# Kernel tuning notes

Hardware: AMD Instinct MI355X
Metric: run time of the kernel (lower is better)

The kernel has to match this reference:

```python
import jax, jax.numpy as jnp
import numpy as np

Lx, Ly, D, P = 4, 5, 4, 2
DEPTH = 5
TAU = 0.1
N = Lx * Ly
B = 64


def setup_inputs() -> dict:
    key = jax.random.key(0)
    k1, k2, k3 = jax.random.split(key, 3)
    # PEPS site tensors: [Lx, Ly, phys, up, down, left, right]; boundary bonds sliced to dim 1 at use.
    peps = jax.random.normal(k1, (Lx, Ly, P, D, D, D, D), dtype=jnp.float32) * 0.5
    # Two-site Trotter gate: expm(-tau * h) for a random symmetric two-body term h (4x4).
    h = jax.random.normal(k2, (4, 4), dtype=jnp.float32)
    h = 0.5 * (h + h.T)
    w, v = jnp.linalg.eigh(h)
    gate = (v * jnp.exp(-TAU * w)) @ v.T  # [4,4]
    x = jax.random.randint(k3, (B, N), 0, 2, dtype=jnp.int32)
    return {"x": x, "peps": peps, "gate": gate}


def _slice_boundary(site, i, j):
    # site: [p, u, d, l, r]; open boundary -> bond dim 1 on lattice edges
    if i == 0:
        site = site[:, :1]
    if i == Lx - 1:
        site = site[:, :, :1]
    if j == 0:
        site = site[:, :, :, :1]
    if j == Ly - 1:
        site = site[..., :1]
    return site


def _peps_statevector(peps):
    # Exact contraction of the open-boundary PEPS to the full 2^N statevector.
    rows = []
    for i in range(Lx):
        T = jnp.ones((1, 1, 1, 1), dtype=peps.dtype)  # [Pphys, Uup, Ddown, l]
        for j in range(Ly):
            s = _slice_boundary(peps[i, j], i, j)
            T = jnp.einsum('PUDl,pudlr->PpUuDdr', T, s)
            Pn, p, U, u, Dn, d, r = T.shape
            T = T.reshape(Pn * p, U * u, Dn * d, r)
        rows.append(T[..., 0])  # [2^Ly, up_bonds, down_bonds]
    S = jnp.ones((1, 1), dtype=peps.dtype)  # [Pphys, down_bonds]
    for row in rows:
        S = jnp.einsum('PU,QUD->PQD', S, row)
        a, b, c = S.shape
        S = S.reshape(a * b, c)
    return S[:, 0]  # [2^N]


def _apply_gate(psi, g, a, b):
    # g: [2,2,2,2] = gate[o1,o2,i1,i2]; psi: (2,)*N
    out = jnp.tensordot(g, psi, axes=([2, 3], [a, b]))
    return jnp.moveaxis(out, (0, 1), (a, b))


def _bonds():
    horiz = [((i, j), (i, j + 1)) for i in range(Lx) for j in range(Ly - 1)]
    vert = [((i, j), (i + 1, j)) for i in range(Lx - 1) for j in range(Ly)]
    return horiz + vert


def reference(x, peps, gate):
    psi = _peps_statevector(peps).reshape((2,) * N)
    g = gate.reshape(2, 2, 2, 2)
    bonds = _bonds()
    for _ in range(DEPTH):
        for (i1, j1), (i2, j2) in bonds:
            psi = _apply_gate(psi, g, i1 * Ly + j1, i2 * Ly + j2)
    psi = psi.reshape(-1)
    pw = 2 ** jnp.arange(N - 1, -1, -1, dtype=jnp.int32)
    idx = (x * pw).sum(axis=1)
    return psi[idx]  # [B] amplitudes
```

## Files before the change

kernel.cpp:

```cpp
#include <hip/hip_runtime.h>


#define PAD(i) ((i) + (((i) >> 4) << 2))
#define PIDX(i,j,p,u,d,l,r) (((((((i)*5+(j))*2+(p))*4+(u))*4+(d))*4+(l))*4+(r))

typedef float v4f __attribute__((ext_vector_type(4)));

static constexpr int COL0  = 0;
static constexpr int COL1  = 4096;
static constexpr int COL2  = COL1 + 1048576;
static constexpr int COL3  = COL2 + 1048576;
static constexpr int COL4  = COL3 + 1048576;
static constexpr int M01TO = COL4 + 4096;
static constexpr int M34TO = M01TO + 65536;
static constexpr int T12TO = M34TO + 65536;
static constexpr int PSIO  = T12TO + 1048576;
static constexpr int CNTO  = PSIO + 1048576;

__device__ __forceinline__ float agl(const float* p) {
  return __hip_atomic_load(p, __ATOMIC_RELAXED, __HIP_MEMORY_SCOPE_AGENT);
}
__device__ __forceinline__ void cohload1(const float* p, v4f& a) {
  asm volatile("global_load_dwordx4 %0, %1, off sc0 sc1"
               : "=&v"(a) : "v"(p) : "memory");
}
__device__ __forceinline__ void cohload2(const float* p0, const float* p1,
                                         v4f& a, v4f& b) {
  asm volatile(
      "global_load_dwordx4 %0, %2, off sc0 sc1\n\t"
      "global_load_dwordx4 %1, %3, off sc0 sc1\n\t"
      "s_waitcnt vmcnt(0)"
      : "=&v"(a), "=&v"(b)
      : "v"(p0), "v"(p1)
      : "memory");
}
__device__ __forceinline__ void cohstore(float* p, v4f v) {
  asm volatile("global_store_dwordx4 %0, %1, off sc0 sc1"
               :
               : "v"(p), "v"(v)
               : "memory");
}
__device__ __forceinline__ void cohstore1(float* p, float v) {
  asm volatile("global_store_dword %0, %1, off sc0 sc1"
               :
               : "v"(p), "v"(v)
               : "memory");
}
__device__ __forceinline__ void vmdrain() {
  asm volatile("s_waitcnt vmcnt(0)" ::: "memory");
}
__device__ __forceinline__ void vmw8() {
  asm volatile("s_waitcnt vmcnt(8)" ::: "memory");
  __builtin_amdgcn_sched_barrier(0);
}
__device__ __forceinline__ void vmw0() {
  asm volatile("s_waitcnt vmcnt(0)" ::: "memory");
  __builtin_amdgcn_sched_barrier(0);
}

__device__ __forceinline__ void gridbar(int* cnts, int gen) {
  vmdrain();
  __syncthreads();
  if (threadIdx.x == 0) {
    int* gc = cnts + (blockIdx.x >> 4) * 64;
    int* root = cnts + 1024;
    int prev = __hip_atomic_fetch_add(gc, 1, __ATOMIC_RELAXED,
                                      __HIP_MEMORY_SCOPE_AGENT);
    if ((prev & 15) == 15)
      __hip_atomic_fetch_add(root, 1, __ATOMIC_RELAXED,
                             __HIP_MEMORY_SCOPE_AGENT);
    while (__hip_atomic_load(root, __ATOMIC_RELAXED,
                             __HIP_MEMORY_SCOPE_AGENT) < gen * 16) {
      __builtin_amdgcn_s_sleep(2);
    }
  }
  __syncthreads();
}

__device__ __forceinline__ void coh_gemm(const float* Bb, const float* Ar,
                                         v4f acc[4]) {
  v4f pa0, pa1, pa2, pa3, pa4, pa5, pa6, pa7;
  v4f pb0, pb1, pb2, pb3, pb4, pb5, pb6, pb7;
#define ISSUE8(buf, base)                                                      \
  cohload1(Bb + ((base) + 0) * 256, buf##0);                                   \
  cohload1(Bb + ((base) + 1) * 256, buf##1);                                   \
  cohload1(Bb + ((base) + 2) * 256, buf##2);                                   \
  cohload1(Bb + ((base) + 3) * 256, buf##3);                                   \
  cohload1(Bb + ((base) + 4) * 256, buf##4);                                   \
  cohload1(Bb + ((base) + 5) * 256, buf##5);                                   \
  cohload1(Bb + ((base) + 6) * 256, buf##6);                                   \
  cohload1(Bb + ((base) + 7) * 256, buf##7)
#define FMA8(buf, base)                                                        \
  {                                                                            \
    _Pragma("unroll") for (int r = 0; r < 4; ++r) {                            \
      acc[r] += buf##0 * Ar[r * 256 + (base) + 0];                             \
      acc[r] += buf##1 * Ar[r * 256 + (base) + 1];                             \
      acc[r] += buf##2 * Ar[r * 256 + (base) + 2];                             \
      acc[r] += buf##3 * Ar[r * 256 + (base) + 3];                             \
      acc[r] += buf##4 * Ar[r * 256 + (base) + 4];                             \
      acc[r] += buf##5 * Ar[r * 256 + (base) + 5];                             \
      acc[r] += buf##6 * Ar[r * 256 + (base) + 6];                             \
      acc[r] += buf##7 * Ar[r * 256 + (base) + 7];                             \
    }                                                                          \
  }
  ISSUE8(pa, 0);
#pragma unroll
  for (int cp = 0; cp < 16; ++cp) {
    ISSUE8(pb, cp * 16 + 8);
    vmw8();
    FMA8(pa, cp * 16);
    if (cp < 15) {
      ISSUE8(pa, cp * 16 + 16);
      vmw8();
    } else {
      vmw0();
    }
    FMA8(pb, cp * 16 + 8);
  }
#undef ISSUE8
#undef FMA8
}

__device__ __forceinline__ void stage8k(const float* gsrc, float* lds, int t) {
  v4f v0, v1, v2, v3;
  cohload1(gsrc + (0 * 512 + t) * 4, v0);
  cohload1(gsrc + (1 * 512 + t) * 4, v1);
  cohload1(gsrc + (2 * 512 + t) * 4, v2);
  cohload1(gsrc + (3 * 512 + t) * 4, v3);
  vmw0();
  *(v4f*)&lds[(0 * 512 + t) * 4] = v0;
  *(v4f*)&lds[(1 * 512 + t) * 4] = v1;
  *(v4f*)&lds[(2 * 512 + t) * 4] = v2;
  *(v4f*)&lds[(3 * 512 + t) * 4] = v3;
}

template <int NB, int HI, int LO>
__device__ __forceinline__ void gate2(float* x, const float* __restrict__ g) {
  constexpr int H = 1 << HI, L = 1 << LO, N = 1 << NB;
#pragma unroll
  for (int o = 0; o < N; ++o) {
    if (o & (H | L)) continue;
    float v0 = x[o], v1 = x[o + L], v2 = x[o + H], v3 = x[o + H + L];
    x[o]         = g[0]  * v0 + g[1]  * v1 + g[2]  * v2 + g[3]  * v3;
    x[o + L]     = g[4]  * v0 + g[5]  * v1 + g[6]  * v2 + g[7]  * v3;
    x[o + H]     = g[8]  * v0 + g[9]  * v1 + g[10] * v2 + g[11] * v3;
    x[o + H + L] = g[12] * v0 + g[13] * v1 + g[14] * v2 + g[15] * v3;
  }
}

template <int ST>
__device__ __forceinline__ void vxf(float* s, const float* __restrict__ g, int b) {
  float x[16];
#pragma unroll
  for (int m = 0; m < 16; ++m) x[m] = s[PAD(b + m * ST)];
  gate2<4, 3, 2>(x, g);
  gate2<4, 2, 1>(x, g);
  gate2<4, 1, 0>(x, g);
#pragma unroll
  for (int m = 0; m < 16; ++m) s[PAD(b + m * ST)] = x[m];
}

template <int B2, int B1, int B0>
__device__ __forceinline__ void bondpair(float* s, const float* __restrict__ g,
                                         int t) {
  constexpr int MASK = (1 << B2) | (1 << B1) | (1 << B0);
  int b = 0, rem = t;
#pragma unroll
  for (int p = 0; p < 12; ++p) {
    if (!((MASK >> p) & 1)) {
      b |= (rem & 1) << p;
      rem >>= 1;
    }
  }
  float x[8];
#pragma unroll
  for (int m = 0; m < 8; ++m) {
    int off = ((m >> 2) & 1) * (1 << B2) + ((m >> 1) & 1) * (1 << B1) +
              (m & 1) * (1 << B0);
    x[m] = s[PAD(b + off)];
  }
  gate2<3, 2, 1>(x, g);
  gate2<3, 1, 0>(x, g);
#pragma unroll
  for (int m = 0; m < 8; ++m) {
    int off = ((m >> 2) & 1) * (1 << B2) + ((m >> 1) & 1) * (1 << B1) +
              (m & 1) * (1 << B0);
    s[PAD(b + off)] = x[m];
  }
}

__global__ __launch_bounds__(512) void k_all(const float* __restrict__ peps,
                                             const int* __restrict__ x,
                                             const float* __restrict__ gate,
                                             float* __restrict__ ws,
                                             float* __restrict__ out,
                                             int* __restrict__ cnt) {
  __shared__ float sm[12320];
  const int t = threadIdx.x;
  const int b = blockIdx.x;
  const int cg = t & 63;
  float* psi = ws + PSIO;
  int gen = 0;

  if (b < 192) {
    float* p01 = sm;
    float* p23 = sm + 4096;
    int col = 1 + (b >> 6);
    int pb = b & 63;
#pragma unroll
    for (int k = 0; k < 8; ++k) {
      int e = k * 512 + t;
      int r12 = e & 15, l12 = (e >> 4) & 15, d2 = (e >> 8) & 3, p = e >> 10;
      int l1 = l12 >> 2, l2 = l12 & 3, r1 = r12 >> 2, r2 = r12 & 3;
      float s01 = 0.f, s23 = 0.f;
#pragma unroll
      for (int d = 0; d < 4; ++d) {
        s01 += peps[PIDX(0, col, (p >> 1), 0, d, l1, r1)] *
               peps[PIDX(1, col, (p & 1), d, d2, l2, r2)];
        s23 += peps[PIDX(2, col, (p >> 1), d2, d, l1, r1)] *
               peps[PIDX(3, col, (p & 1), d, 0, l2, r2)];
      }
      p01[e] = s01;
      p23[e] = s23;
    }
    __syncthreads();
    const int coloffs[3] = {COL1, COL2, COL3};
    float* outc = ws + coloffs[col - 1];
#pragma unroll
    for (int pp = 0; pp < 2; ++pp) {
      int part = pb * 2 + pp;
#pragma unroll
      for (int k = 0; k < 4; ++k) {
        int eq = part * 8192 + (k * 512 + t) * 4;
        int r34b = eq & 15;
        int r12 = (eq >> 4) & 15, l34 = (eq >> 8) & 15, l12 = (eq >> 12) & 15;
        int p = eq >> 16;
        int pa = p >> 2, pbv = p & 3;
        v4f acc = {0.f, 0.f, 0.f, 0.f};
#pragma unroll
        for (int d2 = 0; d2 < 4; ++d2) {
          float a01 = p01[((((pa * 4 + d2) << 4) | l12) << 4) | r12];
          const float4 b4 =
              *(const float4*)&p23[((((pbv * 4 + d2) << 4) | l34) << 4) | r34b];
          acc.x += a01 * b4.x;
          acc.y += a01 * b4.y;
          acc.z += a01 * b4.z;
          acc.w += a01 * b4.w;
        }
        cohstore(&outc[eq], acc);
      }
    }
  } else if (b < 194) {
    float* p01 = sm;
    float* p23 = sm + 4096;
    int col = (b == 192) ? 0 : 4;
    const int lsh = (col == 0) ? 0 : 2;
    const int rsh = (col == 4) ? 0 : 2;
    const int ldim = 1 << lsh, rdim = 1 << rsh;
    const int LLB = 2 * lsh, RRB = 2 * rsh;
    const int LL = 1 << LLB, RR = 1 << RRB;
    int n12 = (LL * RR) << 4;
    for (int e = t; e < n12; e += 512) {
      int r12 = e & (RR - 1);
      int l12 = (e >> RRB) & (LL - 1);
      int d2 = (e >> (RRB + LLB)) & 3;
      int p = e >> (RRB + LLB + 2);
      int l1 = l12 >> lsh, l2 = l12 & (ldim - 1);
      int r1 = r12 >> rsh, r2 = r12 & (rdim - 1);
      float s01 = 0.f, s23 = 0.f;
      for (int d = 0; d < 4; ++d) {
        s01 += peps[PIDX(0, col, (p >> 1), 0, d, l1, r1)] *
               peps[PIDX(1, col, (p & 1), d, d2, l2, r2)];
        s23 += peps[PIDX(2, col, (p >> 1), d2, d, l1, r1)] *
               peps[PIDX(3, col, (p & 1), d, 0, l2, r2)];
      }
      p01[e] = s01;
      p23[e] = s23;
    }
    __syncthreads();
    const int LB = 2 * LLB, RB = 2 * RRB;
    int total = 16 << (LB + RB);
    float* outc = ws + ((col == 0) ? COL0 : COL4);
    for (int e = t; e < total; e += 512) {
      int r = e & ((1 << RB) - 1);
      int l = (e >> RB) & ((1 << LB) - 1);
      int p = e >> (RB + LB);
      int r34 = r & (RR - 1), r12 = r >> RRB;
      int l34 = l & (LL - 1), l12 = l >> LLB;
      int pa = p >> 2, pbv = p & 3;
      float sacc = 0.f;
      for (int d2 = 0; d2 < 4; ++d2) {
        sacc += p01[((((pa * 4 + d2) << LLB) | l12) << RRB) | r12] *
                p23[((((pbv * 4 + d2) << LLB) | l34) << RRB) | r34];
      }
      cohstore1(&outc[e], sacc);
    }
  }
  gridbar(cnt, ++gen);

  {
    float* c3buf = sm;
    float* c4buf = sm + 4112;
    float* col0l = sm + 8224;
    const float* col3 = ws + COL3;
    const float* col4 = ws + COL4;
    const float* col0g = ws + COL0;
    const int L3 = b;
    if (t < 256) {
      float v3[16], v4[16];
#pragma unroll
      for (int k = 0; k < 16; ++k) {
        v4[k] = agl(&col4[k * 256 + t]);
        v3[k] = agl(&col3[k * 65536 + L3 * 256 + t]);
      }
#pragma unroll
      for (int k = 0; k < 16; ++k) {
        c4buf[k * 257 + t] = v4[k];
        c3buf[k * 257 + t] = v3[k];
      }
    } else if (b < 16) {
      int tt = t - 256;
#pragma unroll
      for (int k = 0; k < 16; ++k) col0l[k * 256 + tt] = agl(&col0g[k * 256 + tt]);
    }
    __syncthreads();
    if (t < 256) {
      int c3 = t >> 4, c4 = t & 15;
      float acc = 0.f;
      for (int B = 0; B < 256; ++B)
        acc += c3buf[c3 * 257 + B] * c4buf[c4 * 257 + B];
      cohstore1(&(ws + M34TO)[L3 * 256 + t], acc);
    } else if (b < 16) {
      int rg = (t >> 6) & 3;
      v4f acc[4] = {};
      coh_gemm(ws + COL1 + b * 65536 + cg * 4, &col0l[rg * 4 * 256], acc);
      float* m01p = ws + M01TO;
#pragma unroll
      for (int r = 0; r < 4; ++r)
        cohstore(&m01p[((rg * 4 + r) * 16 + b) * 256 + cg * 4], acc[r]);
    }
  }
  gridbar(cnt, ++gen);

  if (b < 128) {
    float* A = sm;
    int c2 = b & 15, hb = b >> 4;
    stage8k(ws + M01TO + hb * 8192, A, t);
    __syncthreads();
    int rg = t >> 6;
    v4f acc[4] = {};
    coh_gemm(ws + COL2 + c2 * 65536 + cg * 4, &A[rg * 4 * 256], acc);
    float* t012p = ws + T12TO;
#pragma unroll
    for (int r = 0; r < 4; ++r)
      cohstore(&t012p[c2 * 65536 + (hb * 32 + rg * 4 + r) * 256 + cg * 4],
               acc[r]);
  }
  gridbar(cnt, ++gen);

  if (b < 128) {
    float* A = sm;
    float* S = sm;
    {
      v4f v0, v1, v2, v3;
      const float* t012p = ws + T12TO;
      int f0 = (0 * 512 + t) * 4, f1 = (1 * 512 + t) * 4;
      int f2 = (2 * 512 + t) * 4, f3 = (3 * 512 + t) * 4;
      cohload1(t012p + (((f0 >> 8) & 15) * 65536 + (2 * b + (f0 >> 12)) * 256 +
                        (f0 & 255)), v0);
      cohload1(t012p + (((f1 >> 8) & 15) * 65536 + (2 * b + (f1 >> 12)) * 256 +
                        (f1 & 255)), v1);
      cohload1(t012p + (((f2 >> 8) & 15) * 65536 + (2 * b + (f2 >> 12)) * 256 +
                        (f2 & 255)), v2);
      cohload1(t012p + (((f3 >> 8) & 15) * 65536 + (2 * b + (f3 >> 12)) * 256 +
                        (f3 & 255)), v3);
      vmw0();
      *(v4f*)&A[f0] = v0;
      *(v4f*)&A[f1] = v1;
      *(v4f*)&A[f2] = v2;
      *(v4f*)&A[f3] = v3;
    }
    __syncthreads();
    int rg = t >> 6;
    v4f acc[4] = {};
    coh_gemm(ws + M34TO + cg * 4, &A[rg * 4 * 256], acc);
    __syncthreads();
#pragma unroll
    for (int r = 0; r < 4; ++r) {
      int ri = rg * 4 + r;
      int sb = (ri >> 4) * 4112 + (ri & 15) * 257 + cg * 4;
      S[sb + 0] = acc[r].x;
      S[sb + 1] = acc[r].y;
      S[sb + 2] = acc[r].z;
      S[sb + 3] = acc[r].w;
    }
    __syncthreads();
    int tid = t & 255, tgl = t >> 8;
    int c3 = tid >> 4, c2v = tid & 15;
    int tg = 2 * b + tgl;
    int base = c3 * 65536 + (tg >> 4) * 256 + (tg & 15) * 16 + c2v;
#pragma unroll
    for (int v = 0; v < 16; ++v)
      cohstore1(&psi[base + v * 4096], S[tgl * 4112 + c2v * 257 + c3 * 16 + v]);
  }
  gridbar(cnt, ++gen);

  float g[16];
#pragma unroll
  for (int i = 0; i < 16; ++i) g[i] = gate[i];
  float* s = sm;

  for (int it = 0; it < 5; ++it) {
    {
      int f0 = t * 4, f1 = (512 + t) * 4;
      v4f a, c;
      cohload2(psi + b * 4096 + f0, psi + b * 4096 + f1, a, c);
      *(v4f*)(s + PAD(f0)) = a;
      *(v4f*)(s + PAD(f1)) = c;
    }
    __syncthreads();
    bondpair<8, 4, 0>(s, g, t);
    __syncthreads();
    bondpair<9, 5, 1>(s, g, t);
    __syncthreads();
    bondpair<10, 6, 2>(s, g, t);
    __syncthreads();
    bondpair<11, 7, 3>(s, g, t);
    __syncthreads();
    if (t < 256) vxf<256>(s, g, t);
    __syncthreads();
    if (t < 256) vxf<16>(s, g, ((t >> 4) << 8) | (t & 15));
    __syncthreads();
    {
      int f0 = t * 4, f1 = (512 + t) * 4;
      cohstore(psi + b * 4096 + f0, *(const v4f*)(s + PAD(f0)));
      cohstore(psi + b * 4096 + f1, *(const v4f*)(s + PAD(f1)));
    }
    gridbar(cnt, ++gen);

    {
      int f0 = t * 4, f1 = (512 + t) * 4;
      int a0 = (f0 >> 8) * 65536 + ((f0 >> 4) & 15) * 4096 + b * 16 + (f0 & 15);
      int a1 = (f1 >> 8) * 65536 + ((f1 >> 4) & 15) * 4096 + b * 16 + (f1 & 15);
      v4f a, c;
      cohload2(psi + a0, psi + a1, a, c);
      *(v4f*)(s + PAD(f0)) = a;
      *(v4f*)(s + PAD(f1)) = c;
    }
    __syncthreads();
    bondpair<0, 8, 4>(s, g, t);
    __syncthreads();
    bondpair<1, 9, 5>(s, g, t);
    __syncthreads();
    bondpair<2, 10, 6>(s, g, t);
    __syncthreads();
    bondpair<3, 11, 7>(s, g, t);
    __syncthreads();
    if (t < 256) vxf<1>(s, g, t * 16);
    __syncthreads();
    if (t < 256) vxf<256>(s, g, t);
    __syncthreads();
    if (t < 256) vxf<16>(s, g, ((t >> 4) << 8) | (t & 15));
    __syncthreads();
    if (it == 4) {
      if (t < 64) {
        int idx = 0;
#pragma unroll
        for (int q = 0; q < 20; ++q) {
          int i = q / 5, j = q % 5;
          int pos = (j == 0) ? (11 - i)
                   : (j == 1) ? (7 - i)
                   : (j == 2) ? (3 - i)
                   : (j == 3) ? (19 - i)
                              : (15 - i);
          idx |= x[t * 20 + q] << pos;
        }
        if (((idx >> 4) & 255) == b) {
          int local = ((idx >> 16) & 15) * 256 + ((idx >> 12) & 15) * 16 +
                      (idx & 15);
          out[t] = s[PAD(local)];
        }
      }
    } else {
      int f0 = t * 4, f1 = (512 + t) * 4;
      int a0 = (f0 >> 8) * 65536 + ((f0 >> 4) & 15) * 4096 + b * 16 + (f0 & 15);
      int a1 = (f1 >> 8) * 65536 + ((f1 >> 4) & 15) * 4096 + b * 16 + (f1 & 15);
      cohstore(psi + a0, *(const v4f*)(s + PAD(f0)));
      cohstore(psi + a1, *(const v4f*)(s + PAD(f1)));
      gridbar(cnt, ++gen);
    }
  }
}

extern "C" void kernel_launch(void* const* d_in, const int* in_sizes, int n_in,
                              void* d_out, int out_size, void* d_ws, size_t ws_size,
                              hipStream_t stream) {
  const int* x = (const int*)d_in[0];
  const float* peps = (const float*)d_in[1];
  const float* gate = (const float*)d_in[2];
  float* ws = (float*)d_ws;
  float* out = (float*)d_out;
  int* cnt = (int*)(ws + CNTO);

  hipMemsetAsync((void*)cnt, 0, 1088 * sizeof(int), stream);

  k_all<<<256, 512, 0, stream>>>(peps, x, gate, ws, out, cnt);
}
```

Before: 212.9 us.

## Spread contraction GEMM stages across all blocks with smaller output tiles

Reworks the M01, T012 and final psi-assembly stages so that every block in the grid takes part, where before only 16 or 128 blocks did. The M01 stage becomes a per-block LDS dot-product using a staged slice of column 1. The later GEMMs use a new two-row-per-thread variant with vectorized LDS reads and padded strides, and psi is written with vector stores. The aim is to cut idle blocks and per-block serial GEMM length between grid barriers, at the cost of more redundant staging loads and more LDS per block.

```diff
diff --git a/kernel.cpp b/kernel.cpp
--- a/kernel.cpp
+++ b/kernel.cpp
@@ -77,8 +77,9 @@
   __syncthreads();
 }
 
-__device__ __forceinline__ void coh_gemm(const float* Bb, const float* Ar,
-                                         v4f acc[4]) {
+__device__ __forceinline__ void coh_gemm2(const float* Bb, const float* Ar0,
+                                          const float* Ar1, v4f& acc0,
+                                          v4f& acc1) {
   v4f pa0, pa1, pa2, pa3, pa4, pa5, pa6, pa7;
   v4f pb0, pb1, pb2, pb3, pb4, pb5, pb6, pb7;
 #define ISSUE8(buf, base)                                                      \
@@ -92,16 +93,18 @@
   cohload1(Bb + ((base) + 7) * 256, buf##7)
 #define FMA8(buf, base)                                                        \
   {                                                                            \
-    _Pragma("unroll") for (int r = 0; r < 4; ++r) {                            \
-      acc[r] += buf##0 * Ar[r * 256 + (base) + 0];                             \
-      acc[r] += buf##1 * Ar[r * 256 + (base) + 1];                             \
-      acc[r] += buf##2 * Ar[r * 256 + (base) + 2];                             \
-      acc[r] += buf##3 * Ar[r * 256 + (base) + 3];                             \
-      acc[r] += buf##4 * Ar[r * 256 + (base) + 4];                             \
-      acc[r] += buf##5 * Ar[r * 256 + (base) + 5];                             \
-      acc[r] += buf##6 * Ar[r * 256 + (base) + 6];                             \
-      acc[r] += buf##7 * Ar[r * 256 + (base) + 7];                             \
-    }                                                                          \
+    v4f A0a = *(const v4f*)&Ar0[(base)];                                       \
+    v4f A0b = *(const v4f*)&Ar0[(base) + 4];                                   \
+    v4f A1a = *(const v4f*)&Ar1[(base)];                                       \
+    v4f A1b = *(const v4f*)&Ar1[(base) + 4];                                   \
+    acc0 += buf##0 * A0a.x;  acc1 += buf##0 * A1a.x;                           \
+    acc0 += buf##1 * A0a.y;  acc1 += buf##1 * A1a.y;                           \
+    acc0 += buf##2 * A0a.z;  acc1 += buf##2 * A1a.z;                           \
+    acc0 += buf##3 * A0a.w;  acc1 += buf##3 * A1a.w;                           \
+    acc0 += buf##4 * A0b.x;  acc1 += buf##4 * A1b.x;                           \
+    acc0 += buf##5 * A0b.y;  acc1 += buf##5 * A1b.y;                           \
+    acc0 += buf##6 * A0b.z;  acc1 += buf##6 * A1b.z;                           \
+    acc0 += buf##7 * A0b.w;  acc1 += buf##7 * A1b.w;                           \
   }
   ISSUE8(pa, 0);
 #pragma unroll
@@ -121,19 +124,6 @@
 #undef FMA8
 }
 
-__device__ __forceinline__ void stage8k(const float* gsrc, float* lds, int t) {
-  v4f v0, v1, v2, v3;
-  cohload1(gsrc + (0 * 512 + t) * 4, v0);
-  cohload1(gsrc + (1 * 512 + t) * 4, v1);
-  cohload1(gsrc + (2 * 512 + t) * 4, v2);
-  cohload1(gsrc + (3 * 512 + t) * 4, v3);
-  vmw0();
-  *(v4f*)&lds[(0 * 512 + t) * 4] = v0;
-  *(v4f*)&lds[(1 * 512 + t) * 4] = v1;
-  *(v4f*)&lds[(2 * 512 + t) * 4] = v2;
-  *(v4f*)&lds[(3 * 512 + t) * 4] = v3;
-}
-
 template <int NB, int HI, int LO>
 __device__ __forceinline__ void gate2(float* x, const float* __restrict__ g) {
   constexpr int H = 1 << HI, L = 1 << LO, N = 1 << NB;
@@ -195,10 +185,9 @@
                                              float* __restrict__ ws,
                                              float* __restrict__ out,
                                              int* __restrict__ cnt) {
-  __shared__ float sm[12320];
+  __shared__ float sm[16640];
   const int t = threadIdx.x;
   const int b = blockIdx.x;
-  const int cg = t & 63;
   float* psi = ws + PSIO;
   int gen = 0;
 
@@ -302,10 +291,11 @@
     float* c3buf = sm;
     float* c4buf = sm + 4112;
     float* col0l = sm + 8224;
+    float* s1c   = sm + 12384;
     const float* col3 = ws + COL3;
     const float* col4 = ws + COL4;
-    const float* col0g = ws + COL0;
     const int L3 = b;
+    const int c1 = b >> 4, q = b & 15;
     if (t < 256) {
       float v3[16], v4[16];
 #pragma unroll
@@ -318,10 +308,27 @@
         c4buf[k * 257 + t] = v4[k];
         c3buf[k * 257 + t] = v3[k];
       }
-    } else if (b < 16) {
+    } else {
       int tt = t - 256;
-#pragma unroll
-      for (int k = 0; k < 16; ++k) col0l[k * 256 + tt] = agl(&col0g[k * 256 + tt]);
+      const float* col0g = ws + COL0;
+#pragma unroll
+      for (int k = 0; k < 16; ++k)
+        col0l[k * 260 + tt] = agl(&col0g[k * 256 + tt]);
+      const float* c1p = ws + COL1 + c1 * 65536 + tt * 256 + q * 16;
+      v4f w0, w1, w2, w3;
+      cohload1(c1p + 0, w0);
+      cohload1(c1p + 4, w1);
+      cohload1(c1p + 8, w2);
+      cohload1(c1p + 12, w3);
+      vmw0();
+#pragma unroll
+      for (int j = 0; j < 4; ++j) s1c[(0 * 4 + j) * 260 + tt] = w0[j];
+#pragma unroll
+      for (int j = 0; j < 4; ++j) s1c[(1 * 4 + j) * 260 + tt] = w1[j];
+#pragma unroll
+      for (int j = 0; j < 4; ++j) s1c[(2 * 4 + j) * 260 + tt] = w2[j];
+#pragma unroll
+      for (int j = 0; j < 4; ++j) s1c[(3 * 4 + j) * 260 + tt] = w3[j];
     }
     __syncthreads();
     if (t < 256) {
@@ -330,78 +337,111 @@
       for (int B = 0; B < 256; ++B)
         acc += c3buf[c3 * 257 + B] * c4buf[c4 * 257 + B];
       cohstore1(&(ws + M34TO)[L3 * 256 + t], acc);
-    } else if (b < 16) {
-      int rg = (t >> 6) & 3;
-      v4f acc[4] = {};
-      coh_gemm(ws + COL1 + b * 65536 + cg * 4, &col0l[rg * 4 * 256], acc);
-      float* m01p = ws + M01TO;
-#pragma unroll
-      for (int r = 0; r < 4; ++r)
-        cohstore(&m01p[((rg * 4 + r) * 16 + b) * 256 + cg * 4], acc[r]);
+    } else {
+      int tt = t - 256;
+      int c0 = tt >> 4, rc = tt & 15;
+      float acc = 0.f;
+#pragma unroll
+      for (int R = 0; R < 256; R += 4) {
+        v4f a4 = *(const v4f*)&col0l[c0 * 260 + R];
+        v4f s4 = *(const v4f*)&s1c[rc * 260 + R];
+        acc += a4.x * s4.x + a4.y * s4.y + a4.z * s4.z + a4.w * s4.w;
+      }
+      cohstore1(&(ws + M01TO)[(c0 * 16 + c1) * 256 + q * 16 + rc], acc);
     }
   }
   gridbar(cnt, ++gen);
 
-  if (b < 128) {
+  {
     float* A = sm;
-    int c2 = b & 15, hb = b >> 4;
-    stage8k(ws + M01TO + hb * 8192, A, t);
-    __syncthreads();
-    int rg = t >> 6;
-    v4f acc[4] = {};
-    coh_gemm(ws + COL2 + c2 * 65536 + cg * 4, &A[rg * 4 * 256], acc);
+    int c2 = b >> 4, tile = (b >> 2) & 3, qr = b & 3;
+    const float* src = ws + M01TO + tile * 16384;
+    {
+      v4f v0, v1, v2, v3, v4, v5, v6, v7;
+      cohload1(src + (0 * 512 + t) * 4, v0);
+      cohload1(src + (1 * 512 + t) * 4, v1);
+      cohload1(src + (2 * 512 + t) * 4, v2);
+      cohload1(src + (3 * 512 + t) * 4, v3);
+      cohload1(src + (4 * 512 + t) * 4, v4);
+      cohload1(src + (5 * 512 + t) * 4, v5);
+      cohload1(src + (6 * 512 + t) * 4, v6);
+      cohload1(src + (7 * 512 + t) * 4, v7);
+      vmw0();
+#define PUT(k, vv)                                                             \
+  {                                                                            \
+    int f = (k * 512 + t) * 4;                                                 \
+    *(v4f*)&A[(f >> 8) * 260 + (f & 255)] = vv;                                \
+  }
+      PUT(0, v0) PUT(1, v1) PUT(2, v2) PUT(3, v3)
+      PUT(4, v4) PUT(5, v5) PUT(6, v6) PUT(7, v7)
+#undef PUT
+    }
+    __syncthreads();
+    int cg = t & 15, rg = t >> 4;
+    v4f acc0 = {0.f, 0.f, 0.f, 0.f}, acc1 = {0.f, 0.f, 0.f, 0.f};
+    coh_gemm2(ws + COL2 + c2 * 65536 + qr * 64 + cg * 4, &A[(rg * 2) * 260],
+              &A[(rg * 2 + 1) * 260], acc0, acc1);
     float* t012p = ws + T12TO;
-#pragma unroll
-    for (int r = 0; r < 4; ++r)
-      cohstore(&t012p[c2 * 65536 + (hb * 32 + rg * 4 + r) * 256 + cg * 4],
-               acc[r]);
+    int row0 = tile * 64 + rg * 2;
+    cohstore(&t012p[c2 * 65536 + row0 * 256 + qr * 64 + cg * 4], acc0);
+    cohstore(&t012p[c2 * 65536 + (row0 + 1) * 256 + qr * 64 + cg * 4], acc1);
   }
   gridbar(cnt, ++gen);
 
-  if (b < 128) {
+  {
     float* A = sm;
+    int tgq = b >> 2, cq = b & 3;
+    const float* t012p = ws + T12TO;
+    {
+      v4f v0, v1, v2, v3, v4, v5, v6, v7;
+#define SRC(k)                                                                 \
+  (t012p + (((k * 512 + t) * 4 >> 8) & 15) * 65536 +                           \
+   (tgq * 4 + ((k * 512 + t) * 4 >> 12)) * 256 + ((k * 512 + t) * 4 & 255))
+      cohload1(SRC(0), v0);
+      cohload1(SRC(1), v1);
+      cohload1(SRC(2), v2);
+      cohload1(SRC(3), v3);
+      cohload1(SRC(4), v4);
+      cohload1(SRC(5), v5);
+      cohload1(SRC(6), v6);
+      cohload1(SRC(7), v7);
+#undef SRC
+      vmw0();
+#define PUT(k, vv)                                                             \
+  {                                                                            \
+    int f = (k * 512 + t) * 4;                                                 \
+    *(v4f*)&A[(f >> 8) * 260 + (f & 255)] = vv;                                \
+  }
+      PUT(0, v0) PUT(1, v1) PUT(2, v2) PUT(3, v3)
+      PUT(4, v4) PUT(5, v5) PUT(6, v6) PUT(7, v7)
+#undef PUT
+    }
+    __syncthreads();
+    int cg = t & 15, rg = t >> 4;
+    v4f acc0 = {0.f, 0.f, 0.f, 0.f}, acc1 = {0.f, 0.f, 0.f, 0.f};
+    coh_gemm2(ws + M34TO + cq * 64 + cg * 4, &A[(rg * 2) * 260],
+              &A[(rg * 2 + 1) * 260], acc0, acc1);
+    __syncthreads();
     float* S = sm;
-    {
-      v4f v0, v1, v2, v3;
-      const float* t012p = ws + T12TO;
-      int f0 = (0 * 512 + t) * 4, f1 = (1 * 512 + t) * 4;
-      int f2 = (2 * 512 + t) * 4, f3 = (3 * 512 + t) * 4;
-      cohload1(t012p + (((f0 >> 8) & 15) * 65536 + (2 * b + (f0 >> 12)) * 256 +
-                        (f0 & 255)), v0);
-      cohload1(t012p + (((f1 >> 8) & 15) * 65536 + (2 * b + (f1 >> 12)) * 256 +
-                        (f1 & 255)), v1);
-      cohload1(t012p + (((f2 >> 8) & 15) * 65536 + (2 * b + (f2 >> 12)) * 256 +
-                        (f2 & 255)), v2);
-      cohload1(t012p + (((f3 >> 8) & 15) * 65536 + (2 * b + (f3 >> 12)) * 256 +
-                        (f3 & 255)), v3);
-      vmw0();
-      *(v4f*)&A[f0] = v0;
-      *(v4f*)&A[f1] = v1;
-      *(v4f*)&A[f2] = v2;
-      *(v4f*)&A[f3] = v3;
-    }
-    __syncthreads();
-    int rg = t >> 6;
-    v4f acc[4] = {};
-    coh_gemm(ws + M34TO + cg * 4, &A[rg * 4 * 256], acc);
-    __syncthreads();
-#pragma unroll
-    for (int r = 0; r < 4; ++r) {
-      int ri = rg * 4 + r;
-      int sb = (ri >> 4) * 4112 + (ri & 15) * 257 + cg * 4;
-      S[sb + 0] = acc[r].x;
-      S[sb + 1] = acc[r].y;
-      S[sb + 2] = acc[r].z;
-      S[sb + 3] = acc[r].w;
-    }
-    __syncthreads();
-    int tid = t & 255, tgl = t >> 8;
-    int c3 = tid >> 4, c2v = tid & 15;
-    int tg = 2 * b + tgl;
-    int base = c3 * 65536 + (tg >> 4) * 256 + (tg & 15) * 16 + c2v;
-#pragma unroll
-    for (int v = 0; v < 16; ++v)
-      cohstore1(&psi[base + v * 4096], S[tgl * 4112 + c2v * 257 + c3 * 16 + v]);
+    *(v4f*)&S[(rg * 2 + 0) * 68 + cg * 4] = acc0;
+    *(v4f*)&S[(rg * 2 + 1) * 68 + cg * 4] = acc1;
+    __syncthreads();
+#pragma unroll
+    for (int k = 0; k < 2; ++k) {
+      int idx = k * 512 + t;
+      int c2g = idx & 3, c4 = (idx >> 2) & 15, c3l = (idx >> 6) & 3;
+      int tgi = (idx >> 8) & 3;
+      int tg = tgq * 4 + tgi;
+      int col = c3l * 16 + c4;
+      v4f v;
+      v.x = S[(tgi * 16 + c2g * 4 + 0) * 68 + col];
+      v.y = S[(tgi * 16 + c2g * 4 + 1) * 68 + col];
+      v.z = S[(tgi * 16 + c2g * 4 + 2) * 68 + col];
+      v.w = S[(tgi * 16 + c2g * 4 + 3) * 68 + col];
+      int addr = (cq * 4 + c3l) * 65536 + c4 * 4096 + (tg >> 4) * 256 +
+                 (tg & 15) * 16 + c2g * 4;
+      cohstore(&psi[addr], v);
+    }
   }
   gridbar(cnt, ++gen);
 
```

New measurement: 206.7 us. -2.9%, faster.
